# Kernel optimization log

Hardware: AMD Instinct MI355X
Metric: run time of the kernel (lower is better)

Reference implementation:

```python
import jax, jax.numpy as jnp
import numpy as np

N_NODES = 48758  # hardcoded in the original DAN.forward
EPS_BN = 1e-5


def setup_inputs() -> dict:
    key = jax.random.key(0)
    ks = jax.random.split(key, 14)
    E, D, R, L, NI = 780000, 128, 4, 2, 10000
    sc = 1.0 / np.sqrt(D)
    inp = {
        "x": jax.random.normal(ks[0], (N_NODES, D), jnp.float32),
        "edge_index": jax.random.randint(ks[1], (2, E), 0, N_NODES),
        "idx": jax.random.randint(ks[2], (NI,), 0, N_NODES),
        "edge_type": jax.random.randint(ks[3], (E,), 0, R),
        "edge_weight": jax.random.uniform(ks[4], (E,), jnp.float32),
        # RiskGNN params
        "proj_w": jax.random.normal(ks[5], (D, D), jnp.float32) * sc,
        "proj_b": jax.random.normal(ks[6], (D,), jnp.float32) * 0.01,
        "bn_g": jnp.ones((D,), jnp.float32),
        "bn_b": jnp.zeros((D,), jnp.float32),
        # per-layer DAN params, stacked over L=2 layers (same dims)
        "win_w": jax.random.normal(ks[7], (L, D, D), jnp.float32) * sc,
        "win_b": jax.random.normal(ks[8], (L, D), jnp.float32) * 0.01,
        "wrel": jax.random.normal(ks[9], (L, R, D, D), jnp.float32) * sc,
        "out_w": jax.random.normal(ks[10], (L, D, D), jnp.float32) * sc,
        "out_b": jax.random.normal(ks[11], (L, D), jnp.float32) * 0.01,
    }
    return inp


def _dan_layer(h, edge_index, edge_type, rel_num, win_w, win_b, wrel, out_w, out_b):
    dst = edge_index[0]
    src = edge_index[1]
    x = h @ win_w + win_b                       # [N, D]
    x_j = x[src]                                # edge gather [E, D]
    # gcn_norm(add_self_loops=False): deg over col (=src axis edge_index[1])
    ones_e = jnp.ones(dst.shape[0], x.dtype)
    deg = jax.ops.segment_sum(ones_e, src, num_segments=N_NODES)
    dinv = jnp.where(deg > 0, jax.lax.rsqrt(jnp.maximum(deg, 1.0)), 0.0)
    norm_w = (dinv[dst] * dinv[src])[:, None]   # [E, 1]
    msg_gcn = jax.ops.segment_sum(x_j * norm_w, dst, num_segments=N_NODES)
    # per-relation masked matmul (unsorted grouped GEMM)
    res = jnp.zeros_like(x_j)
    for r in range(rel_num):
        res = jnp.where((edge_type == r)[:, None], x_j @ wrel[r], res)
    # segment softmax over edges grouped by dst, per channel
    seg_max = jax.ops.segment_max(res, dst, num_segments=N_NODES)
    ex = jnp.exp(res - seg_max[dst])
    denom = jax.ops.segment_sum(ex, dst, num_segments=N_NODES)
    weig = ex / denom[dst]
    msg = jax.ops.segment_sum(res * weig, dst, num_segments=N_NODES)
    out = (msg_gcn + 0.1 * jax.nn.relu(msg)) @ out_w + out_b
    return out


def reference(x, edge_weight, proj_w, proj_b, bn_g, bn_b, win_w, win_b, wrel,
              out_w, out_b, edge_index, edge_type, idx):
    rel_num = wrel.shape[1]
    n_layer = win_w.shape[0]
    h = x @ proj_w + proj_b
    # BatchNorm1d (training-mode batch stats, biased var)
    mu = jnp.mean(h, axis=0)
    var = jnp.mean((h - mu) ** 2, axis=0)
    h = (h - mu) * jax.lax.rsqrt(var + EPS_BN) * bn_g + bn_b
    h = jax.nn.relu(h)
    for i in range(n_layer):
        h = _dan_layer(h, edge_index, edge_type, rel_num,
                       win_w[i], win_b[i], wrel[i], out_w[i], out_b[i])
    h = jax.nn.gelu(h, approximate=False)  # dropout is identity at eval
    return h[idx]
```

## Files before the change

kernel.cpp:

```cpp
#include <hip/hip_runtime.h>
#include <hip/hip_bf16.h>
#include <math.h>

#define D 128
#define DD (128 * 128)
#define RS 640
#define CAPB 4608

typedef __attribute__((ext_vector_type(8))) short short8;
typedef __attribute__((ext_vector_type(4))) float f32x4;

__device__ __forceinline__ float bf2f(unsigned short u) {
    union { unsigned int i; float f; } x; x.i = ((unsigned int)u) << 16; return x.f;
}
__device__ __forceinline__ unsigned short f2bf(float f) {
    unsigned int i = __float_as_uint(f);
    unsigned int r = (i + 0x7FFFu + ((i >> 16) & 1u)) >> 16;
    return (unsigned short)r;
}

__device__ __forceinline__ int vote_flag(const unsigned short* __restrict__ x) {
    __shared__ int bad_s;
    if (threadIdx.x == 0) bad_s = 0;
    __syncthreads();
    unsigned int e = (x[threadIdx.x] >> 7) & 0xFFu;
    unsigned long long b = __ballot(e < 100u || e > 140u);
    if ((threadIdx.x & 63) == 0) atomicAdd(&bad_s, __popcll(b));
    __syncthreads();
    return bad_s > 48 ? 1 : 0;
}

__global__ __launch_bounds__(256) void k_stage1(
    const void* __restrict__ xin, unsigned short* __restrict__ xb, int n4, int nbx, int nbw,
    const void* s0, const void* s1, const void* s2, const void* s3,
    const void* s4, const void* s5, const void* s6, const void* s7, const void* s8,
    int o1, int o2, int o3, int o4, int o5, int o6, int o7, int o8,
    int total, unsigned short* __restrict__ wdst,
    const int* __restrict__ ei, const int* __restrict__ et, int E,
    unsigned int* __restrict__ cd_g, unsigned int* __restrict__ cs_g,
    uint2* __restrict__ ebuck, unsigned short* __restrict__ sbuck)
{
    int bx = blockIdx.x, t = threadIdx.x;
    if (bx < nbx) {
        int fl = vote_flag((const unsigned short*)xin);
        int i = bx * 256 + t;
        if (i >= n4) return;
        if (fl) {
            float4 v = ((const float4*)xin)[i];
            uint2 o;
            o.x = (unsigned int)f2bf(v.x) | ((unsigned int)f2bf(v.y) << 16);
            o.y = (unsigned int)f2bf(v.z) | ((unsigned int)f2bf(v.w) << 16);
            ((uint2*)xb)[i] = o;
        } else {
            ((uint2*)xb)[i] = ((const uint2*)xin)[i];
        }
    } else if (bx < nbx + nbw) {
        int fl = vote_flag((const unsigned short*)xin);
        int i = (bx - nbx) * 256 + t;
        if (i >= total) return;
        const void* src; int base;
        if      (i < o1) { src = s0; base = 0;  }
        else if (i < o2) { src = s1; base = o1; }
        else if (i < o3) { src = s2; base = o2; }
        else if (i < o4) { src = s3; base = o3; }
        else if (i < o5) { src = s4; base = o4; }
        else if (i < o6) { src = s5; base = o5; }
        else if (i < o7) { src = s6; base = o6; }
        else if (i < o8) { src = s7; base = o7; }
        else             { src = s8; base = o8; }
        int li = i - base;
        wdst[i] = fl ? f2bf(((const float*)src)[li]) : ((const unsigned short*)src)[li];
    } else {
        __shared__ unsigned int hd[256], hs[256];
        int b = bx - nbx - nbw;
        hd[t] = 0u; hs[t] = 0u;
        unsigned int d8[8], sp8[8];
        __syncthreads();
        int base = b * 2048;
        #pragma unroll
        for (int i = 0; i < 8; ++i) {
            int e = base + t + i * 256;
            if (e < E) {
                unsigned int d = (unsigned int)ei[e];
                unsigned int s = (unsigned int)ei[E + e];
                unsigned int tt = (unsigned int)et[e];
                d8[i] = d; sp8[i] = s | (tt << 16);
                atomicAdd(&hd[d >> 8], 1u);
                atomicAdd(&hs[s >> 8], 1u);
            } else d8[i] = 0xFFFFFFFFu;
        }
        __syncthreads();
        hd[t] = atomicAdd(&cd_g[t], hd[t]);
        hs[t] = atomicAdd(&cs_g[t], hs[t]);
        __syncthreads();
        #pragma unroll
        for (int i = 0; i < 8; ++i) {
            if (d8[i] != 0xFFFFFFFFu) {
                unsigned int bk = d8[i] >> 8;
                unsigned int pos = atomicAdd(&hd[bk], 1u);
                if (pos < (unsigned)CAPB) ebuck[(size_t)bk * CAPB + pos] = make_uint2(d8[i], sp8[i]);
                unsigned int s = sp8[i] & 0xFFFFu;
                unsigned int bk2 = s >> 8;
                unsigned int pos2 = atomicAdd(&hs[bk2], 1u);
                if (pos2 < (unsigned)CAPB) sbuck[(size_t)bk2 * CAPB + pos2] = (unsigned short)s;
            }
        }
    }
}

__device__ __forceinline__ void gemm_core(
    const unsigned short* __restrict__ A, const unsigned short* __restrict__ W,
    unsigned short* As, unsigned short* Wt, f32x4 (&acc)[2][8])
{
    int t = threadIdx.x;
    #pragma unroll
    for (int i = 0; i < 8; ++i) {
        int ch = t + i * 256;
        int row = ch >> 4;
        int kc  = ch & 15;
        uint4 v = *((const uint4*)(A + (size_t)row * D + kc * 8));
        *((uint4*)&As[row * 128 + (kc ^ (row & 15)) * 8]) = v;
    }
    #pragma unroll
    for (int i = 0; i < 8; ++i) {
        int ch = t + i * 256;
        int k  = ch >> 4;
        int n0 = (ch & 15) * 8;
        uint4 v = *((const uint4*)(W + k * D + n0));
        const unsigned short* pv = (const unsigned short*)&v;
        int kc = k >> 3, ko = k & 7;
        #pragma unroll
        for (int j = 0; j < 8; ++j) {
            int n = n0 + j;
            Wt[n * 128 + ((kc ^ (n & 15)) * 8) + ko] = pv[j];
        }
    }
    __syncthreads();
    int wave = t >> 6, lane = t & 63, quad = lane >> 4, l16 = lane & 15;
    int rowbase = wave * 32;
    #pragma unroll
    for (int a = 0; a < 2; ++a)
        #pragma unroll
        for (int b = 0; b < 8; ++b) acc[a][b] = (f32x4){0.f, 0.f, 0.f, 0.f};
    #pragma unroll
    for (int ks = 0; ks < 4; ++ks) {
        int chunk = ks * 4 + quad;
        short8 af[2], bf[8];
        #pragma unroll
        for (int rt = 0; rt < 2; ++rt) {
            int r = rowbase + rt * 16 + l16;
            af[rt] = *((const short8*)&As[r * 128 + (chunk ^ (r & 15)) * 8]);
        }
        #pragma unroll
        for (int ct = 0; ct < 8; ++ct) {
            int n = ct * 16 + l16;
            bf[ct] = *((const short8*)&Wt[n * 128 + (chunk ^ (n & 15)) * 8]);
        }
        #pragma unroll
        for (int rt = 0; rt < 2; ++rt)
            #pragma unroll
            for (int ct = 0; ct < 8; ++ct)
                acc[rt][ct] = __builtin_amdgcn_mfma_f32_16x16x32_bf16(af[rt], bf[ct], acc[rt][ct], 0, 0, 0);
    }
}

__device__ __forceinline__ void store_transposed(f32x4 (&acc)[2][8], unsigned short* dst)
{
    int t = threadIdx.x;
    int wave = t >> 6, lane = t & 63, quad = lane >> 4, l16 = lane & 15;
    int rowbase = wave * 32;
    #pragma unroll
    for (int rt = 0; rt < 2; ++rt) {
        #pragma unroll
        for (int ct = 0; ct < 8; ++ct) {
            int n = ct * 16 + l16;
            #pragma unroll
            for (int r = 0; r < 4; ++r) {
                int k = rowbase + rt * 16 + quad * 4 + r;
                dst[n * 128 + (((k >> 3) ^ (n & 15)) * 8) + (k & 7)] = f2bf(acc[rt][ct][r]);
            }
        }
    }
}

__global__ __launch_bounds__(256) void k_stage2(
    const unsigned int* __restrict__ cd_g, const uint2* __restrict__ ebuck,
    unsigned int* __restrict__ rp, unsigned int* __restrict__ pckd,
    const unsigned int* __restrict__ cs_g, const unsigned short* __restrict__ sbuck,
    float* __restrict__ dinv, int N, int NB,
    const unsigned short* __restrict__ wbase, unsigned short* __restrict__ bc,
    unsigned short* __restrict__ wtg, unsigned short* __restrict__ wraw,
    unsigned short* __restrict__ bxl1, int o4, int o5, int o6, int o7, int o8)
{
    __shared__ __align__(16) char pool[65536];
    int bx = blockIdx.x, t = threadIdx.x;
    if (bx < NB) {
        uint2* ebuf = (uint2*)pool;
        unsigned int* bins = (unsigned int*)(pool + CAPB * 8);
        unsigned int* gsum = bins + 1024;
        unsigned int* csc  = gsum + 256;
        int b = bx;
        unsigned int cvt_ = (t < NB) ? min(cd_g[t], (unsigned)CAPB) : 0u;
        csc[t] = cvt_;
        __syncthreads();
        for (int off = 1; off < 256; off <<= 1) {
            unsigned int v = csc[t];
            unsigned int a = (t >= off) ? csc[t - off] : 0u;
            __syncthreads();
            csc[t] = v + a;
            __syncthreads();
        }
        unsigned int cnt = min(cd_g[b], (unsigned)CAPB);
        unsigned int beg = csc[b] - cnt;
        #pragma unroll
        for (int j = 0; j < 4; ++j) bins[t + j * 256] = 0u;
        __syncthreads();
        for (unsigned int i = t; i < cnt; i += 256) {
            uint2 v = ebuck[(size_t)b * CAPB + i];
            ebuf[i] = v;
            atomicAdd(&bins[((v.x & 255u) << 2) | ((v.y >> 16) & 3u)], 1u);
        }
        __syncthreads();
        unsigned int b0 = bins[4 * t], b1 = bins[4 * t + 1], b2 = bins[4 * t + 2], b3 = bins[4 * t + 3];
        unsigned int s4 = b0 + b1 + b2 + b3;
        gsum[t] = s4;
        __syncthreads();
        for (int off = 1; off < 256; off <<= 1) {
            unsigned int v = gsum[t];
            unsigned int a = (t >= off) ? gsum[t - off] : 0u;
            __syncthreads();
            gsum[t] = v + a;
            __syncthreads();
        }
        unsigned int base0 = gsum[t] - s4;
        bins[4 * t]     = beg + base0;
        bins[4 * t + 1] = beg + base0 + b0;
        bins[4 * t + 2] = beg + base0 + b0 + b1;
        bins[4 * t + 3] = beg + base0 + b0 + b1 + b2;
        int n = (b << 8) + t;
        if (n <= N) rp[n] = beg + base0;
        __syncthreads();
        for (unsigned int i = t; i < cnt; i += 256) {
            uint2 v = ebuf[i];
            unsigned int key = ((v.x & 255u) << 2) | ((v.y >> 16) & 3u);
            unsigned int pos = atomicAdd(&bins[key], 1u);
            pckd[pos] = v.y;
        }
    } else if (bx < 2 * NB) {
        unsigned int* bins = (unsigned int*)pool;
        int b = bx - NB;
        unsigned int cnt = min(cs_g[b], (unsigned)CAPB);
        bins[t] = 0u;
        __syncthreads();
        for (unsigned int i = t; i < cnt; i += 256)
            atomicAdd(&bins[sbuck[(size_t)b * CAPB + i] & 255u], 1u);
        __syncthreads();
        int n = (b << 8) + t;
        if (n < N) {
            unsigned int dg = bins[t];
            dinv[n] = dg ? rsqrtf((float)dg) : 0.f;
        }
    } else if (bx < 2 * NB + 4) {
        int r = bx - 2 * NB;
        const unsigned short* A = wbase + o4;
        const unsigned short* W = wbase + o6 + (size_t)r * DD;
        f32x4 acc[2][8];
        gemm_core(A, W, (unsigned short*)pool, (unsigned short*)pool + DD, acc);
        store_transposed(acc, wtg + (size_t)(3 + r) * DD);
        const unsigned short* b_in0 = wbase + o5;
        if (t < 128) {
            float s = 0.f;
            for (int k = 0; k < 128; ++k)
                s += bf2f(b_in0[k]) * bf2f(W[k * D + t]);
            bc[r * D + t] = f2bf(s);
        }
    } else if (bx == 2 * NB + 4) {
        const unsigned short* A = wbase + o7;
        const unsigned short* W = wbase + o4 + DD;
        f32x4 acc[2][8];
        gemm_core(A, W, (unsigned short*)pool, (unsigned short*)pool + DD, acc);
        store_transposed(acc, wtg + (size_t)2 * DD);
        int wave = t >> 6, lane = t & 63, quad = lane >> 4, l16 = lane & 15;
        int rowbase = wave * 32;
        #pragma unroll
        for (int rt = 0; rt < 2; ++rt)
            #pragma unroll
            for (int ct = 0; ct < 8; ++ct) {
                int col = ct * 16 + l16;
                #pragma unroll
                for (int r = 0; r < 4; ++r) {
                    int row = rowbase + rt * 16 + quad * 4 + r;
                    wraw[row * 128 + col] = f2bf(acc[rt][ct][r]);
                }
            }
        const unsigned short* b_out0 = wbase + o8;
        const unsigned short* b_in1  = wbase + o5 + D;
        if (t < 128) {
            float s = bf2f(b_in1[t]);
            for (int k = 0; k < 128; ++k)
                s += bf2f(b_out0[k]) * bf2f(W[k * D + t]);
            bxl1[t] = f2bf(s);
        }
    } else {
        int pb = bx - 2 * NB - 5;
        int mi = pb >> 3, sub = pb & 7;
        const unsigned short* src;
        int m;
        if (mi == 0)      { src = wbase;            m = 0;  }
        else if (mi == 1) { src = wbase + o4;       m = 1;  }
        else              { src = wbase + o7 + DD;  m = 12; }
        int c = sub * 256 + t;
        int n = c >> 4, kc = c & 15;
        unsigned short tmp[8];
        #pragma unroll
        for (int ko = 0; ko < 8; ++ko) tmp[ko] = src[(kc * 8 + ko) * 128 + n];
        *((uint4*)(wtg + (size_t)m * DD + n * 128 + ((kc ^ (n & 15)) * 8))) = *(uint4*)tmp;
    }
}

__global__ __launch_bounds__(256) void k_stage2b(
    const unsigned short* __restrict__ wraw, const unsigned short* __restrict__ wbase,
    const unsigned short* __restrict__ bxl1, unsigned short* __restrict__ bc,
    unsigned short* __restrict__ wtg, int o6)
{
    __shared__ __align__(16) unsigned short pool[2 * DD];
    int r = blockIdx.x, t = threadIdx.x;
    const unsigned short* W = wbase + o6 + (size_t)(4 + r) * DD;
    f32x4 acc[2][8];
    gemm_core(wraw, W, pool, pool + DD, acc);
    store_transposed(acc, wtg + (size_t)(7 + r) * DD);
    if (t < 128) {
        float s = 0.f;
        for (int k = 0; k < 128; ++k)
            s += bf2f(bxl1[k]) * bf2f(W[k * D + t]);
        bc[(4 + r) * D + t] = f2bf(s);
    }
}

__device__ __forceinline__ void load_afrag(
    const unsigned short* __restrict__ A, int M, int blockRow, short8 (&af)[2][4])
{
    int t = threadIdx.x;
    int wave = t >> 6, lane = t & 63, quad = lane >> 4, l16 = lane & 15;
    int rowbase = blockRow + wave * 32;
    int r0 = min(rowbase + l16, M - 1);
    int r1 = min(rowbase + 16 + l16, M - 1);
    const unsigned short* a0 = A + (size_t)r0 * D;
    const unsigned short* a1 = A + (size_t)r1 * D;
    #pragma unroll
    for (int ks = 0; ks < 4; ++ks) {
        int chunk = ks * 4 + quad;
        af[0][ks] = *((const short8*)(a0 + chunk * 8));
        af[1][ks] = *((const short8*)(a1 + chunk * 8));
    }
}

__device__ __forceinline__ void mfma_slice(
    const unsigned short* Wt, short8 (&af)[2][4], f32x4 (&acc)[2][8])
{
    int lane = threadIdx.x & 63, quad = lane >> 4, l16 = lane & 15;
    #pragma unroll
    for (int a = 0; a < 2; ++a)
        #pragma unroll
        for (int b = 0; b < 8; ++b) acc[a][b] = (f32x4){0.f, 0.f, 0.f, 0.f};
    #pragma unroll
    for (int ks = 0; ks < 4; ++ks) {
        int chunk = ks * 4 + quad;
        short8 bf[8];
        #pragma unroll
        for (int ct = 0; ct < 8; ++ct)
            bf[ct] = *((const short8*)&Wt[(ct * 16 + l16) * 128 + ((chunk ^ l16) * 8)]);
        #pragma unroll
        for (int rt = 0; rt < 2; ++rt)
            #pragma unroll
            for (int ct = 0; ct < 8; ++ct)
                acc[rt][ct] = __builtin_amdgcn_mfma_f32_16x16x32_bf16(af[rt][ks], bf[ct], acc[rt][ct], 0, 0, 0);
    }
}

__device__ __forceinline__ void gemm_core_fast(
    const unsigned short* __restrict__ A, const unsigned short* __restrict__ Wt_g,
    int M, int blockRow, unsigned short* Wt, f32x4 (&acc)[2][8])
{
    int t = threadIdx.x;
    #pragma unroll
    for (int i = 0; i < 8; ++i)
        ((uint4*)Wt)[t + i * 256] = ((const uint4*)Wt_g)[t + i * 256];
    short8 af[2][4];
    load_afrag(A, M, blockRow, af);
    __syncthreads();
    mfma_slice(Wt, af, acc);
}

__global__ __launch_bounds__(256) void gemm_proj(
    const unsigned short* __restrict__ A, const unsigned short* __restrict__ Wt_g,
    const unsigned short* __restrict__ bias, unsigned short* __restrict__ C,
    int M, float* __restrict__ psum, float* __restrict__ psq)
{
    __shared__ unsigned short Wt[DD];
    __shared__ float smS[4][128], smQ[4][128];
    f32x4 acc[2][8];
    int blockRow = blockIdx.x * 128;
    gemm_core_fast(A, Wt_g, M, blockRow, Wt, acc);
    int t = threadIdx.x;
    int wave = t >> 6, lane = t & 63, quad = lane >> 4, l16 = lane & 15;
    int rowbase = wave * 32;
    #pragma unroll
    for (int ct = 0; ct < 8; ++ct) {
        int col = ct * 16 + l16;
        float bv = bf2f(bias[col]);
        float ps = 0.f, pq = 0.f;
        #pragma unroll
        for (int rt = 0; rt < 2; ++rt) {
            #pragma unroll
            for (int r = 0; r < 4; ++r) {
                int grow = blockRow + rowbase + rt * 16 + quad * 4 + r;
                if (grow < M) {
                    float v = acc[rt][ct][r] + bv;
                    C[(size_t)grow * D + col] = f2bf(v);
                    ps += v; pq += v * v;
                }
            }
        }
        ps += __shfl_xor(ps, 16, 64); ps += __shfl_xor(ps, 32, 64);
        pq += __shfl_xor(pq, 16, 64); pq += __shfl_xor(pq, 32, 64);
        if (quad == 0) { smS[wave][col] = ps; smQ[wave][col] = pq; }
    }
    __syncthreads();
    if (t < 128) {
        psum[blockIdx.x * 128 + t] = smS[0][t] + smS[1][t] + smS[2][t] + smS[3][t];
        psq[blockIdx.x * 128 + t]  = smQ[0][t] + smQ[1][t] + smQ[2][t] + smQ[3][t];
    }
}

__global__ __launch_bounds__(256) void k_bnstats(
    const float* __restrict__ psum, const float* __restrict__ psq,
    int nb, int N, const unsigned short* __restrict__ g,
    const unsigned short* __restrict__ b,
    float* __restrict__ scale, float* __restrict__ shift)
{
    int col = blockIdx.x, t = threadIdx.x;
    float s = 0.f, q = 0.f;
    for (int i = t; i < nb; i += 256) {
        s += psum[i * 128 + col];
        q += psq[i * 128 + col];
    }
    #pragma unroll
    for (int o = 32; o >= 1; o >>= 1) {
        s += __shfl_xor(s, o, 64);
        q += __shfl_xor(q, o, 64);
    }
    __shared__ float sS[4], sQ[4];
    if ((t & 63) == 0) { sS[t >> 6] = s; sQ[t >> 6] = q; }
    __syncthreads();
    if (t == 0) {
        s = sS[0] + sS[1] + sS[2] + sS[3];
        q = sQ[0] + sQ[1] + sQ[2] + sQ[3];
        float inv = 1.f / (float)N;
        float mean = s * inv;
        float var = fmaxf(q * inv - mean * mean, 0.f);
        float sc = rsqrtf(var + 1e-5f) * bf2f(g[col]);
        scale[col] = sc;
        shift[col] = bf2f(b[col]) - mean * sc;
    }
}

__global__ __launch_bounds__(256) void gemm_fused(
    const unsigned short* __restrict__ h, const unsigned short* __restrict__ wtg,
    const unsigned short* __restrict__ b_in_l, const unsigned short* __restrict__ bc_l,
    unsigned char* __restrict__ xy8, const float* __restrict__ dinv,
    const float* __restrict__ bnsc, const float* __restrict__ bnsh, int M, int l)
{
    __shared__ unsigned short Wt[DD];
    f32x4 acc[2][8];
    int slice = blockIdx.y;
    int m = (slice == 0) ? (1 + l) : (3 + l * 4 + slice - 1);
    int blockRow = blockIdx.x * 128;
    int t = threadIdx.x;
    const unsigned short* Wt_g = wtg + (size_t)m * DD;
    #pragma unroll
    for (int i = 0; i < 8; ++i)
        ((uint4*)Wt)[t + i * 256] = ((const uint4*)Wt_g)[t + i * 256];
    short8 af[2][4];
    load_afrag(h, M, blockRow, af);
    if (bnsc) {
        int quad = (t & 63) >> 4;
        #pragma unroll
        for (int rt = 0; rt < 2; ++rt)
            #pragma unroll
            for (int ks = 0; ks < 4; ++ks) {
                int ch0 = (ks * 4 + quad) * 8;
                unsigned short* p = (unsigned short*)&af[rt][ks];
                #pragma unroll
                for (int j = 0; j < 8; ++j) {
                    float f = bf2f(p[j]);
                    f = fmaxf(fmaf(f, bnsc[ch0 + j], bnsh[ch0 + j]), 0.f);
                    p[j] = f2bf(f);
                }
            }
    }
    __syncthreads();
    mfma_slice(Wt, af, acc);

    int wave = t >> 6, lane = t & 63, quad = lane >> 4, l16 = lane & 15;
    int rowbase = wave * 32;
    int boff = (slice == 0) ? 0 : (128 + (slice - 1) * 128);
    #pragma unroll
    for (int rt = 0; rt < 2; ++rt) {
        float dv[4];
        if (slice == 0) {
            #pragma unroll
            for (int r = 0; r < 4; ++r) {
                int grow = min(blockRow + rowbase + rt * 16 + quad * 4 + r, M - 1);
                dv[r] = dinv[grow];
            }
        }
        #pragma unroll
        for (int ct = 0; ct < 8; ++ct) {
            int col = ct * 16 + l16;
            float bv = (slice == 0) ? bf2f(b_in_l[col]) : bf2f(bc_l[(slice - 1) * D + col]);
            #pragma unroll
            for (int r = 0; r < 4; ++r) {
                int grow = blockRow + rowbase + rt * 16 + quad * 4 + r;
                if (grow < M) {
                    float v = acc[rt][ct][r] + bv;
                    if (slice == 0) v *= dv[r];
                    int p = __builtin_amdgcn_cvt_pk_fp8_f32(v, v, 0, false);
                    xy8[(size_t)grow * RS + boff + col] = (unsigned char)(p & 0xFF);
                }
            }
        }
    }
}

__global__ __launch_bounds__(256) void gemm_out(
    const unsigned short* __restrict__ zg, const unsigned short* __restrict__ Wt_g,
    const unsigned short* __restrict__ bias, void* __restrict__ out,
    int M, const unsigned short* __restrict__ xprobe)
{
    int fl = vote_flag(xprobe);
    __shared__ unsigned short Wt[DD];
    f32x4 acc[2][8];
    int blockRow = blockIdx.x * 128;
    gemm_core_fast(zg, Wt_g, M, blockRow, Wt, acc);
    int t = threadIdx.x;
    int wave = t >> 6, lane = t & 63, quad = lane >> 4, l16 = lane & 15;
    int rowbase = wave * 32;
    #pragma unroll
    for (int rt = 0; rt < 2; ++rt) {
        #pragma unroll
        for (int ct = 0; ct < 8; ++ct) {
            int col = ct * 16 + l16;
            float bv = bf2f(bias[col]);
            #pragma unroll
            for (int r = 0; r < 4; ++r) {
                int grow = blockRow + rowbase + rt * 16 + quad * 4 + r;
                if (grow < M) {
                    float v = acc[rt][ct][r] + bv;
                    float gl = 0.5f * v * (1.f + erff(v * 0.70710678118654752f));
                    size_t o = (size_t)grow * D + col;
                    if (fl) ((float*)out)[o] = gl;
                    else    ((unsigned short*)out)[o] = f2bf(gl);
                }
            }
        }
    }
}

__device__ __forceinline__ void acc_edge2(uint2 xv, uint2 yv, float vm,
                                          float* g, float* dd, float* ss) {
    const unsigned int* xw = (const unsigned int*)&xv;
    const unsigned int* yw = (const unsigned int*)&yv;
    #pragma unroll
    for (int w = 0; w < 2; ++w) {
        auto xlo = __builtin_amdgcn_cvt_pk_f32_fp8(xw[w], false);
        auto xhi = __builtin_amdgcn_cvt_pk_f32_fp8(xw[w], true);
        auto ylo = __builtin_amdgcn_cvt_pk_f32_fp8(yw[w], false);
        auto yhi = __builtin_amdgcn_cvt_pk_f32_fp8(yw[w], true);
        float vx[4] = {xlo[0], xlo[1], xhi[0], xhi[1]};
        float vy[4] = {ylo[0], ylo[1], yhi[0], yhi[1]};
        int j = 4 * w;
        #pragma unroll
        for (int i = 0; i < 4; ++i) {
            g[j + i] = fmaf(vx[i], vm, g[j + i]);
            float e = __expf(vy[i]);
            dd[j + i] = fmaf(e, vm, dd[j + i]);
            ss[j + i] = fmaf(vy[i] * e, vm, ss[j + i]);
        }
    }
}

__global__ __launch_bounds__(256) void k_edge(
    const unsigned int* __restrict__ rp, const unsigned int* __restrict__ packed,
    const unsigned char* __restrict__ xy8, const float* __restrict__ dinv,
    unsigned short* __restrict__ zout, int NN, const int* __restrict__ nodes)
{
    int lane = threadIdx.x & 63;
    int slot = blockIdx.x * 4 + (threadIdx.x >> 6);
    if (slot >= NN) return;
    int node = nodes ? nodes[slot] : slot;
    node = __builtin_amdgcn_readfirstlane(node);
    unsigned int beg = rp[node], end = rp[node + 1];
    int eg = lane >> 4;
    int cb = (lane & 15) * 8;
    float g[8], dd[8], ss[8];
    #pragma unroll
    for (int j = 0; j < 8; ++j) { g[j] = 0.f; dd[j] = 0.f; ss[j] = 0.f; }

    for (unsigned int e0 = beg; e0 < end; e0 += 8) {
        unsigned int eA = e0 + (unsigned int)eg;
        unsigned int eB = eA + 4u;
        float vmA = (eA < end) ? 1.f : 0.f;
        float vmB = (eB < end) ? 1.f : 0.f;
        unsigned int pA = packed[(eA < end) ? eA : beg];
        unsigned int pB = packed[(eB < end) ? eB : beg];
        unsigned int sA = pA & 0xFFFFu, tA = (pA >> 16) & 3u;
        unsigned int sB = pB & 0xFFFFu, tB = (pB >> 16) & 3u;
        const unsigned char* bA = xy8 + (size_t)sA * RS;
        const unsigned char* bB = xy8 + (size_t)sB * RS;
        uint2 xvA = *((const uint2*)(bA + cb));
        uint2 yvA = *((const uint2*)(bA + 128 + tA * 128 + cb));
        uint2 xvB = *((const uint2*)(bB + cb));
        uint2 yvB = *((const uint2*)(bB + 128 + tB * 128 + cb));
        acc_edge2(xvA, yvA, vmA, g, dd, ss);
        acc_edge2(xvB, yvB, vmB, g, dd, ss);
    }

    #pragma unroll
    for (int j = 0; j < 8; ++j) {
        g[j]  += __shfl_xor(g[j], 16, 64);  g[j]  += __shfl_xor(g[j], 32, 64);
        dd[j] += __shfl_xor(dd[j], 16, 64); dd[j] += __shfl_xor(dd[j], 32, 64);
        ss[j] += __shfl_xor(ss[j], 16, 64); ss[j] += __shfl_xor(ss[j], 32, 64);
    }
    if (eg == 0) {
        float dn = dinv[node];
        unsigned int o[4];
        #pragma unroll
        for (int w = 0; w < 4; ++w) {
            int j0 = w * 2, j1 = w * 2 + 1;
            float m0 = (dd[j0] > 0.f) ? ss[j0] / dd[j0] : 0.f;
            float m1 = (dd[j1] > 0.f) ? ss[j1] / dd[j1] : 0.f;
            float z0 = fmaf(g[j0], dn, 0.1f * fmaxf(m0, 0.f));
            float z1 = fmaf(g[j1], dn, 0.1f * fmaxf(m1, 0.f));
            o[w] = (unsigned int)f2bf(z0) | ((unsigned int)f2bf(z1) << 16);
        }
        *((uint4*)(zout + (size_t)slot * D + cb)) = *(uint4*)o;
    }
}

extern "C" void kernel_launch(void* const* d_in, const int* in_sizes, int n_in,
                              void* d_out, int out_size, void* d_ws, size_t ws_size,
                              hipStream_t stream)
{
    const int* ei  = (const int*)d_in[1];
    const int* idx = (const int*)d_in[2];
    const int* et  = (const int*)d_in[3];
    const unsigned short* xprobe = (const unsigned short*)d_in[0];

    int N  = in_sizes[0] / D;
    int E  = in_sizes[1] / 2;
    int NI = in_sizes[2];
    int L  = in_sizes[9] / (D * D);
    int R  = in_sizes[11] / (L * D * D);

    int NB = (N + 255) >> 8;
    int BA = (E + 2047) / 2048;

    char* ws = (char*)d_ws;
    size_t off = 0;
    auto alloc = [&](size_t bytes) -> char* {
        char* p = ws + off;
        off += (bytes + 255) & ~(size_t)255;
        return p;
    };
    unsigned short* h    = (unsigned short*)alloc((size_t)N * D * 2);
    unsigned char*  xy8  = (unsigned char*)alloc((size_t)N * RS);
    unsigned short* z    = (unsigned short*)alloc((size_t)N * D * 2);
    unsigned short* xb   = (unsigned short*)alloc((size_t)N * D * 2);
    unsigned short* zg   = (unsigned short*)alloc((size_t)NI * D * 2);
    float*          dinv = (float*)alloc((size_t)N * 4);
    unsigned int*   rp   = (unsigned int*)alloc((size_t)(N + 1) * 4);
    unsigned int*   pckd = (unsigned int*)alloc((size_t)E * 4);
    int gb  = (N + 127) / 128;
    float*          psum = (float*)alloc((size_t)gb * 128 * 4);
    float*          psq  = (float*)alloc((size_t)gb * 128 * 4);
    float*          bscale = (float*)alloc(128 * 4);
    float*          bshift = (float*)alloc(128 * 4);
    unsigned int*   cursors = (unsigned int*)alloc(512 * 4);
    unsigned int*   cd_g = cursors;
    unsigned int*   cs_g = cursors + 256;
    uint2*          ebuck = (uint2*)xy8;
    unsigned short* sbuck = (unsigned short*)z;
    int o1 = D * D;
    int o2 = o1 + D;
    int o3 = o2 + D;
    int o4 = o3 + D;
    int o5 = o4 + L * D * D;
    int o6 = o5 + L * D;
    int o7 = o6 + L * R * D * D;
    int o8 = o7 + L * D * D;
    int wt = o8 + L * D;
    unsigned short* wbase  = (unsigned short*)alloc((size_t)wt * 2);
    unsigned short* b_proj = wbase + o1;
    unsigned short* g_bn   = wbase + o2;
    unsigned short* b_bn   = wbase + o3;
    unsigned short* b_in   = wbase + o5;
    unsigned short* b_out  = wbase + o8;
    unsigned short* bc     = (unsigned short*)alloc((size_t)L * R * D * 2);
    unsigned short* wtg    = (unsigned short*)alloc((size_t)13 * DD * 2);
    unsigned short* wraw   = (unsigned short*)alloc((size_t)DD * 2);
    unsigned short* bxl1   = (unsigned short*)alloc((size_t)D * 2);
    (void)ws_size; (void)n_in; (void)out_size;

    int gb2 = (NI + 127) / 128;
    int nb4 = (N + 3) / 4;
    int ni4 = (NI + 3) / 4;
    int n4 = N * D / 4;
    int nbx = (n4 + 255) / 256;
    int nbw = (wt + 255) / 256;

    hipMemsetAsync(cursors, 0, 512 * 4, stream);

    k_stage1<<<nbx + nbw + BA, 256, 0, stream>>>(
        d_in[0], xb, n4, nbx, nbw,
        d_in[5], d_in[6], d_in[7], d_in[8], d_in[9], d_in[10], d_in[11], d_in[12], d_in[13],
        o1, o2, o3, o4, o5, o6, o7, o8, wt, wbase,
        ei, et, E, cd_g, cs_g, ebuck, sbuck);

    k_stage2<<<2 * NB + 5 + 24, 256, 0, stream>>>(
        cd_g, ebuck, rp, pckd, cs_g, sbuck, dinv, N, NB,
        wbase, bc, wtg, wraw, bxl1, o4, o5, o6, o7, o8);

    k_stage2b<<<R, 256, 0, stream>>>(wraw, wbase, bxl1, bc, wtg, o6);

    gemm_proj<<<gb, 256, 0, stream>>>(xb, wtg, b_proj, h, N, psum, psq);
    k_bnstats<<<128, 256, 0, stream>>>(psum, psq, gb, N, g_bn, b_bn, bscale, bshift);

    gemm_fused<<<dim3(gb, 1 + R), 256, 0, stream>>>(h, wtg, b_in, bc, xy8, dinv, bscale, bshift, N, 0);
    k_edge<<<nb4, 256, 0, stream>>>(rp, pckd, xy8, dinv, z, N, nullptr);

    gemm_fused<<<dim3(gb, 1 + R), 256, 0, stream>>>(z, wtg, bxl1, bc + R * D, xy8, dinv, nullptr, nullptr, N, 1);
    k_edge<<<ni4, 256, 0, stream>>>(rp, pckd, xy8, dinv, zg, NI, idx);

    gemm_out<<<gb2, 256, 0, stream>>>(zg, wtg + (size_t)12 * DD, b_out + D, d_out, NI, xprobe);
}
```

Measured before the change: 313.5 us.

## Fold stage2b weight prep into gemm_proj launch and unroll edge gather by four

The separate k_stage2b launch, which builds the composed layer-2 relation weights, is merged into gemm_proj as R extra tail blocks. This removes one kernel launch and its serialization gap. gemm_proj's shared memory grows to hold the larger pool for those blocks, which may lower occupancy for the projection GEMM blocks. Separately, the k_edge loop now handles 16 edges per iteration and issues all packed and row loads before accumulating, to put more independent memory requests in flight at the cost of extra registers.

```diff
diff --git a/kernel.cpp b/kernel.cpp
--- a/kernel.cpp
+++ b/kernel.cpp
@@ -318,25 +318,6 @@
     }
 }
 
-__global__ __launch_bounds__(256) void k_stage2b(
-    const unsigned short* __restrict__ wraw, const unsigned short* __restrict__ wbase,
-    const unsigned short* __restrict__ bxl1, unsigned short* __restrict__ bc,
-    unsigned short* __restrict__ wtg, int o6)
-{
-    __shared__ __align__(16) unsigned short pool[2 * DD];
-    int r = blockIdx.x, t = threadIdx.x;
-    const unsigned short* W = wbase + o6 + (size_t)(4 + r) * DD;
-    f32x4 acc[2][8];
-    gemm_core(wraw, W, pool, pool + DD, acc);
-    store_transposed(acc, wtg + (size_t)(7 + r) * DD);
-    if (t < 128) {
-        float s = 0.f;
-        for (int k = 0; k < 128; ++k)
-            s += bf2f(bxl1[k]) * bf2f(W[k * D + t]);
-        bc[(4 + r) * D + t] = f2bf(s);
-    }
-}
-
 __device__ __forceinline__ void load_afrag(
     const unsigned short* __restrict__ A, int M, int blockRow, short8 (&af)[2][4])
 {
@@ -395,14 +376,33 @@
 __global__ __launch_bounds__(256) void gemm_proj(
     const unsigned short* __restrict__ A, const unsigned short* __restrict__ Wt_g,
     const unsigned short* __restrict__ bias, unsigned short* __restrict__ C,
-    int M, float* __restrict__ psum, float* __restrict__ psq)
-{
-    __shared__ unsigned short Wt[DD];
-    __shared__ float smS[4][128], smQ[4][128];
+    int M, float* __restrict__ psum, float* __restrict__ psq, int gb,
+    const unsigned short* __restrict__ wraw, const unsigned short* __restrict__ wbase,
+    const unsigned short* __restrict__ bxl1, unsigned short* __restrict__ bc,
+    unsigned short* __restrict__ wtg, int o6)
+{
+    __shared__ __align__(16) char pool[2 * DD * 2 + 4096];
+    int t = threadIdx.x;
+    if (blockIdx.x >= gb) {
+        int r = blockIdx.x - gb;
+        const unsigned short* W = wbase + o6 + (size_t)(4 + r) * DD;
+        f32x4 acc[2][8];
+        gemm_core(wraw, W, (unsigned short*)pool, (unsigned short*)pool + DD, acc);
+        store_transposed(acc, wtg + (size_t)(7 + r) * DD);
+        if (t < 128) {
+            float s = 0.f;
+            for (int k = 0; k < 128; ++k)
+                s += bf2f(bxl1[k]) * bf2f(W[k * D + t]);
+            bc[(4 + r) * D + t] = f2bf(s);
+        }
+        return;
+    }
+    unsigned short* Wt = (unsigned short*)pool;
+    float* smS = (float*)(pool + 2 * DD * 2);
+    float* smQ = smS + 512;
     f32x4 acc[2][8];
     int blockRow = blockIdx.x * 128;
     gemm_core_fast(A, Wt_g, M, blockRow, Wt, acc);
-    int t = threadIdx.x;
     int wave = t >> 6, lane = t & 63, quad = lane >> 4, l16 = lane & 15;
     int rowbase = wave * 32;
     #pragma unroll
@@ -424,12 +424,12 @@
         }
         ps += __shfl_xor(ps, 16, 64); ps += __shfl_xor(ps, 32, 64);
         pq += __shfl_xor(pq, 16, 64); pq += __shfl_xor(pq, 32, 64);
-        if (quad == 0) { smS[wave][col] = ps; smQ[wave][col] = pq; }
+        if (quad == 0) { smS[wave * 128 + col] = ps; smQ[wave * 128 + col] = pq; }
     }
     __syncthreads();
     if (t < 128) {
-        psum[blockIdx.x * 128 + t] = smS[0][t] + smS[1][t] + smS[2][t] + smS[3][t];
-        psq[blockIdx.x * 128 + t]  = smQ[0][t] + smQ[1][t] + smQ[2][t] + smQ[3][t];
+        psum[blockIdx.x * 128 + t] = smS[t] + smS[128 + t] + smS[256 + t] + smS[384 + t];
+        psq[blockIdx.x * 128 + t]  = smQ[t] + smQ[128 + t] + smQ[256 + t] + smQ[384 + t];
     }
 }
 
@@ -607,23 +607,26 @@
     #pragma unroll
     for (int j = 0; j < 8; ++j) { g[j] = 0.f; dd[j] = 0.f; ss[j] = 0.f; }
 
-    for (unsigned int e0 = beg; e0 < end; e0 += 8) {
-        unsigned int eA = e0 + (unsigned int)eg;
-        unsigned int eB = eA + 4u;
-        float vmA = (eA < end) ? 1.f : 0.f;
-        float vmB = (eB < end) ? 1.f : 0.f;
-        unsigned int pA = packed[(eA < end) ? eA : beg];
-        unsigned int pB = packed[(eB < end) ? eB : beg];
-        unsigned int sA = pA & 0xFFFFu, tA = (pA >> 16) & 3u;
-        unsigned int sB = pB & 0xFFFFu, tB = (pB >> 16) & 3u;
-        const unsigned char* bA = xy8 + (size_t)sA * RS;
-        const unsigned char* bB = xy8 + (size_t)sB * RS;
-        uint2 xvA = *((const uint2*)(bA + cb));
-        uint2 yvA = *((const uint2*)(bA + 128 + tA * 128 + cb));
-        uint2 xvB = *((const uint2*)(bB + cb));
-        uint2 yvB = *((const uint2*)(bB + 128 + tB * 128 + cb));
-        acc_edge2(xvA, yvA, vmA, g, dd, ss);
-        acc_edge2(xvB, yvB, vmB, g, dd, ss);
+    for (unsigned int e0 = beg; e0 < end; e0 += 16) {
+        unsigned int pk[4];
+        float vm[4];
+        #pragma unroll
+        for (int u = 0; u < 4; ++u) {
+            unsigned int e = e0 + u * 4 + (unsigned int)eg;
+            vm[u] = (e < end) ? 1.f : 0.f;
+            pk[u] = packed[(e < end) ? e : beg];
+        }
+        uint2 xv[4], yv[4];
+        #pragma unroll
+        for (int u = 0; u < 4; ++u) {
+            unsigned int s = pk[u] & 0xFFFFu;
+            unsigned int tt = (pk[u] >> 16) & 3u;
+            const unsigned char* bp = xy8 + (size_t)s * RS;
+            xv[u] = *((const uint2*)(bp + cb));
+            yv[u] = *((const uint2*)(bp + 128 + tt * 128 + cb));
+        }
+        #pragma unroll
+        for (int u = 0; u < 4; ++u) acc_edge2(xv[u], yv[u], vm[u], g, dd, ss);
     }
 
     #pragma unroll
@@ -731,9 +734,8 @@
         cd_g, ebuck, rp, pckd, cs_g, sbuck, dinv, N, NB,
         wbase, bc, wtg, wraw, bxl1, o4, o5, o6, o7, o8);
 
-    k_stage2b<<<R, 256, 0, stream>>>(wraw, wbase, bxl1, bc, wtg, o6);
-
-    gemm_proj<<<gb, 256, 0, stream>>>(xb, wtg, b_proj, h, N, psum, psq);
+    gemm_proj<<<gb + R, 256, 0, stream>>>(xb, wtg, b_proj, h, N, psum, psq, gb,
+                                          wraw, wbase, bxl1, bc, wtg, o6);
     k_bnstats<<<128, 256, 0, stream>>>(psum, psq, gb, N, g_bn, b_bn, bscale, bshift);
 
     gemm_fused<<<dim3(gb, 1 + R), 256, 0, stream>>>(h, wtg, b_in, bc, xy8, dinv, bscale, bshift, N, 0);
```

Result: no change. 312.1 us (-0.5%).
